# Kernel tuning notes

Measured on AMD Instinct MI355X. Metric: run time of the kernel, lower is better.

Reference implementation:

```python
import jax, jax.numpy as jnp
import numpy as np

D_MODEL = 256
N_HEADS = 8
D_HEAD = D_MODEL // N_HEADS
EMB = [16, 16, 16, 16]
CUMSUM = [0, 16, 32, 48, 64]
PSUM = sum(EMB)
LEVELS = [(122, 122), (61, 61), (31, 31), (16, 16)]
S_TOTAL = sum(h * w for h, w in LEVELS)
IMG = 976.0


def swap_pairs(x):
    # swap consecutive pairs along the leading (view) dim
    return x.reshape(-1, 2, *x.shape[1:])[:, ::-1].reshape(x.shape)


def grid_sample_bilinear(img, grid):
    # img: [B, H, W, D]; grid: [B, Q, 2] in [-1, 1]; align_corners=False, zero padding
    B, H, W, D = img.shape
    gx = (grid[..., 0] + 1.0) * (W * 0.5) - 0.5
    gy = (grid[..., 1] + 1.0) * (H * 0.5) - 0.5
    x0 = jnp.floor(gx)
    y0 = jnp.floor(gy)
    wx = (gx - x0)[..., None]
    wy = (gy - y0)[..., None]
    x0i = x0.astype(jnp.int32)
    y0i = y0.astype(jnp.int32)
    flat = img.reshape(B, H * W, D)

    def gather(xi, yi):
        valid = ((xi >= 0) & (xi < W) & (yi >= 0) & (yi < H)).astype(img.dtype)
        idx = jnp.clip(yi, 0, H - 1) * W + jnp.clip(xi, 0, W - 1)
        v = jnp.take_along_axis(flat, idx[..., None], axis=1)
        return v * valid[..., None]

    v00 = gather(x0i, y0i)
    v01 = gather(x0i + 1, y0i)
    v10 = gather(x0i, y0i + 1)
    v11 = gather(x0i + 1, y0i + 1)
    return (v00 * (1 - wx) * (1 - wy) + v01 * wx * (1 - wy)
            + v10 * (1 - wx) * wy + v11 * wx * wy)


def ms_deform_attn_core(value, shapes, sampling_locations, attention_weights):
    # value: [N, S, M, D]; sampling_locations: [N, Lq, M, P, 2]; attention_weights: [N, Lq, M, P]
    N, S, M, D = value.shape
    Lq = sampling_locations.shape[1]
    grids = 2.0 * sampling_locations - 1.0
    outs = []
    start = 0
    for lid, (H, W) in enumerate(shapes):
        p0, p1 = CUMSUM[lid], CUMSUM[lid + 1]
        Pl = p1 - p0
        v = value[:, start:start + H * W].reshape(N, H, W, M, D)
        v = v.transpose(0, 3, 1, 2, 4).reshape(N * M, H, W, D)
        g = grids[:, :, :, p0:p1].transpose(0, 2, 1, 3, 4).reshape(N * M, Lq * Pl, 2)
        outs.append(grid_sample_bilinear(v, g).reshape(N * M, Lq, Pl, D))
        start += H * W
    samp = jnp.concatenate(outs, axis=2)  # [N*M, Lq, Psum, D]
    w = attention_weights.transpose(0, 2, 1, 3).reshape(N * M, Lq, PSUM, 1)
    out = (samp * w).sum(axis=2)  # [N*M, Lq, D]
    return out.reshape(N, M, Lq, D).transpose(0, 2, 1, 3).reshape(N, Lq, M * D)


def _forward(query, input_flatten, reference_points, p_pfws, pt_transforms,
             W_val, b_val, W_attn, b_attn, W_out, b_out, shapes):
    N, Lq, _ = query.shape
    value = (input_flatten @ W_val.T + b_val).reshape(N, -1, N_HEADS, D_HEAD)
    attn = jax.nn.softmax((query @ W_attn.T + b_attn).reshape(N, Lq, N_HEADS, PSUM), axis=-1)

    # reverse 2x3 affine transform on reference points, scale to pixels
    A = pt_transforms[:, :, :2]
    t = pt_transforms[:, :, 2]
    orig = jnp.einsum('nij,nqj->nqi', jnp.linalg.inv(A), reference_points - t[:, None, :]) * IMG

    # epipolar line in the second (swapped) view: point(x) = ts + ms * x, x in [0, IMG]
    P1 = p_pfws
    P2 = swap_pairs(p_pfws)
    A1 = P1[:, :, :3]
    b1 = P1[:, :, 3]
    cam = -jnp.linalg.solve(A1, b1[:, :, None])[:, :, 0]  # camera center [N,3]
    uh = jnp.concatenate([orig, jnp.ones_like(orig[..., :1])], -1)
    ray = jnp.einsum('nij,nqj->nqi', jnp.linalg.inv(A1), uh - b1[:, None, :])  # [N,Q,3]

    def proj2(X):
        Xh = jnp.concatenate([X, jnp.ones_like(X[..., :1])], -1)
        y = jnp.einsum('nij,nqj->nqi', P2, Xh)
        return y[..., :2] / (y[..., 2:3] + 1e-8)

    ts = proj2(jnp.broadcast_to(cam[:, None, :], ray.shape))
    ms = (proj2(ray) - ts) / IMG

    locs = []
    for n_pts in EMB:
        xs = jnp.linspace(0.0, IMG, n_pts)
        locs.append(ts[:, :, None, :] + ms[:, :, None, :] * xs[None, None, :, None])
    loc = jnp.concatenate(locs, axis=2) / IMG  # [N, Lq, Psum, 2]

    T2 = swap_pairs(pt_transforms)
    loc = jnp.einsum('nij,nqpj->nqpi', T2[:, :, :2], loc) + T2[:, :, 2][:, None, None, :]
    loc = jnp.clip(loc, 0.0, 1.0)
    samp_loc = jnp.broadcast_to(loc[:, :, None, :, :], (N, Lq, N_HEADS, PSUM, 2))

    out = ms_deform_attn_core(swap_pairs(value), shapes, samp_loc, attn)
    return out @ W_out.T + b_out


def setup_inputs() -> dict:
    key = jax.random.key(0)
    ks = jax.random.split(key, 12)
    N, Lq = 4, 1000
    query = jax.random.normal(ks[0], (N, Lq, D_MODEL), jnp.float32)
    input_flatten = jax.random.normal(ks[1], (N, S_TOTAL, D_MODEL), jnp.float32)
    reference_points = jax.random.uniform(ks[2], (N, Lq, 2), jnp.float32)
    p_pfws = jnp.asarray(np.eye(3, 4), jnp.float32) + 0.05 * jax.random.normal(ks[3], (N, 3, 4), jnp.float32)
    pt_transforms = jnp.asarray(np.eye(2, 3), jnp.float32) + 0.05 * jax.random.normal(ks[4], (N, 2, 3), jnp.float32)
    W_val = 0.05 * jax.random.normal(ks[5], (D_MODEL, D_MODEL), jnp.float32)
    b_val = jnp.zeros((D_MODEL,), jnp.float32)
    W_attn = 0.05 * jax.random.normal(ks[6], (N_HEADS * PSUM, D_MODEL), jnp.float32)
    b_attn = jnp.zeros((N_HEADS * PSUM,), jnp.float32)
    W_out = 0.05 * jax.random.normal(ks[7], (D_MODEL, D_MODEL), jnp.float32)
    b_out = jnp.zeros((D_MODEL,), jnp.float32)
    input_spatial_shapes = np.asarray(LEVELS, np.int64)
    input_level_start_index = np.asarray(np.cumsum([0] + [h * w for h, w in LEVELS])[:-1], np.int64)
    return {"query": query, "input_flatten": input_flatten, "reference_points": reference_points,
            "p_pfws": p_pfws, "pt_transforms": pt_transforms,
            "W_val": W_val, "b_val": b_val, "W_attn": W_attn, "b_attn": b_attn,
            "W_out": W_out, "b_out": b_out,
            "input_spatial_shapes": input_spatial_shapes,
            "input_level_start_index": input_level_start_index}


def reference(query, input_flatten, reference_points, p_pfws, pt_transforms,
              W_val, b_val, W_attn, b_attn, W_out, b_out,
              input_spatial_shapes, input_level_start_index):
    shapes = [(int(h), int(w)) for h, w in np.asarray(input_spatial_shapes)]
    return _forward(query, input_flatten, reference_points, p_pfws, pt_transforms,
                    W_val, b_val, W_attn, b_attn, W_out, b_out, shapes)
```

## Files before the change

kernel.cpp:

```cpp
#include <hip/hip_runtime.h>
#include <hip/hip_bf16.h>
#include <math.h>

#define NB 4
#define LQ 1000
#define NHEAD 8
#define DHEAD 32
#define DMODEL 256
#define PSUM 64
#define STOT 19822
#define IMGF 976.0f
#define GK 256

__device__ __constant__ int c_LH[4] = {122, 61, 31, 16};
__device__ __constant__ int c_LW[4] = {122, 61, 31, 16};
__device__ __constant__ int c_LST[4] = {0, 14884, 18605, 19566};

typedef __attribute__((ext_vector_type(8))) short bf16x8;
typedef __attribute__((ext_vector_type(4))) float f32x4;

__device__ inline unsigned int pk2(float a, float b) {
    unsigned short ua = __bfloat16_as_ushort(__float2bfloat16(a));
    unsigned short ub = __bfloat16_as_ushort(__float2bfloat16(b));
    return (unsigned int)ua | ((unsigned int)ub << 16);
}
__device__ inline float bf2f(unsigned short u) {
    return __uint_as_float(((unsigned int)u) << 16);
}
__device__ inline bf16x8 cvt8(float4 u, float4 v) {
    union { unsigned int w[4]; bf16x8 h; } r;
    r.w[0] = pk2(u.x, u.y); r.w[1] = pk2(u.z, u.w);
    r.w[2] = pk2(v.x, v.y); r.w[3] = pk2(v.z, v.w);
    return r.h;
}
__device__ inline void gll16(const void* g, void* l) {
    __builtin_amdgcn_global_load_lds(
        (const __attribute__((address_space(1))) void*)g,
        (__attribute__((address_space(3))) void*)l, 16, 0, 0);
}
__device__ inline void hard_barrier() {
    asm volatile("" ::: "memory");
    __builtin_amdgcn_sched_barrier(0);
    __builtin_amdgcn_s_barrier();
    __builtin_amdgcn_sched_barrier(0);
    asm volatile("" ::: "memory");
}

__device__ inline void make_consts(int n, const float* p_pfws, const float* pt,
                                   float* consts) {
    const float* P1 = p_pfws + n * 12;
    const float* P2 = p_pfws + (n ^ 1) * 12;
    const float* T  = pt + n * 6;
    const float* T2 = pt + (n ^ 1) * 6;
    float* C = consts + n * 48;
    float det = T[0]*T[4] - T[1]*T[3];
    float idet = 1.0f/det;
    C[0] =  T[4]*idet; C[1] = -T[1]*idet;
    C[2] = -T[3]*idet; C[3] =  T[0]*idet;
    C[4] = T[2]; C[5] = T[5];
    float a=P1[0], b=P1[1], c=P1[2];
    float d=P1[4], e=P1[5], f=P1[6];
    float g=P1[8], h=P1[9], i=P1[10];
    float b10=P1[3], b11=P1[7], b12=P1[11];
    float A_=e*i-f*h, B_=c*h-b*i, Cc=b*f-c*e;
    float D_=f*g-d*i, E_=a*i-c*g, F_=c*d-a*f;
    float G_=d*h-e*g, H_=b*g-a*h, I_=a*e-b*d;
    float det3 = a*A_ + b*D_ + c*G_;
    float id3 = 1.0f/det3;
    C[6]=A_*id3;  C[7]=B_*id3;  C[8]=Cc*id3;
    C[9]=D_*id3;  C[10]=E_*id3; C[11]=F_*id3;
    C[12]=G_*id3; C[13]=H_*id3; C[14]=I_*id3;
    C[15]=b10; C[16]=b11; C[17]=b12;
    for (int k = 0; k < 12; ++k) C[18+k] = P2[k];
    float cam0 = -(C[6]*b10  + C[7]*b11  + C[8]*b12);
    float cam1 = -(C[9]*b10  + C[10]*b11 + C[11]*b12);
    float cam2 = -(C[12]*b10 + C[13]*b11 + C[14]*b12);
    float y0 = P2[0]*cam0 + P2[1]*cam1 + P2[2]*cam2  + P2[3];
    float y1 = P2[4]*cam0 + P2[5]*cam1 + P2[6]*cam2  + P2[7];
    float y2 = P2[8]*cam0 + P2[9]*cam1 + P2[10]*cam2 + P2[11];
    float inv = 1.0f/(y2 + 1e-8f);
    C[30] = y0*inv; C[31] = y1*inv;
    for (int k = 0; k < 6; ++k) C[32+k] = T2[k];
}

__global__ void prep(const float* __restrict__ Wv, const float* __restrict__ Wa,
                     const float* __restrict__ Wo,
                     unsigned short* __restrict__ wbv, unsigned short* __restrict__ wba,
                     unsigned short* __restrict__ wbo,
                     const float* __restrict__ p_pfws, const float* __restrict__ pt,
                     float* __restrict__ consts) {
    int bid = blockIdx.x;
    if (bid == 256) {
        int n = threadIdx.x;
        if (n < NB) make_consts(n, p_pfws, pt, consts);
        return;
    }
    int i = bid * 256 + threadIdx.x;
    const float* src; unsigned short* dst; int off;
    if (i < 16384)      { src = Wv; dst = wbv; off = i; }
    else if (i < 49152) { src = Wa; dst = wba; off = i - 16384; }
    else                { src = Wo; dst = wbo; off = i - 49152; }
    float4 f = ((const float4*)src)[off];
    ushort4 o;
    o.x = __bfloat16_as_ushort(__float2bfloat16(f.x));
    o.y = __bfloat16_as_ushort(__float2bfloat16(f.y));
    o.z = __bfloat16_as_ushort(__float2bfloat16(f.z));
    o.w = __bfloat16_as_ushort(__float2bfloat16(f.w));
    ((ushort4*)dst)[off] = o;
}

__global__ __launch_bounds__(256, 1)
void gemm_val_regB(const float* __restrict__ X, const unsigned short* __restrict__ Wb,
                   const float* __restrict__ bias, unsigned short* __restrict__ out,
                   int M, int T, int CHUNK) {
    __shared__ __align__(16) char As[2][32768];
    const int tid  = threadIdx.x;
    const int lane = tid & 63;
    const int wq   = tid >> 6;
    const int l15  = lane & 15;
    const int koct = lane >> 4;
    const int t0   = blockIdx.x * CHUNK;
    int nt = T - t0; if (nt > CHUNK) nt = CHUNK;
    if (nt <= 0) return;

    bf16x8 breg[8][4];
    #pragma unroll
    for (int ks = 0; ks < 8; ++ks)
        #pragma unroll
        for (int ni = 0; ni < 4; ++ni) {
            int col = wq * 64 + ni * 16 + l15;
            breg[ks][ni] = *(const bf16x8*)((const char*)Wb + (size_t)col * 512
                                            + ks * 64 + koct * 16);
        }
    float bias_v[4];
    #pragma unroll
    for (int ni = 0; ni < 4; ++ni) bias_v[ni] = bias[wq * 64 + ni * 16 + l15];

#define STAGE(g, b) do {                                                      \
        _Pragma("unroll") for (int j = 0; j < 8; ++j) {                       \
            int r_ = wq * 8 + j;                                              \
            int gr_ = (g) * 32 + r_; if (gr_ >= M) gr_ = M - 1;               \
            int lch_ = lane ^ (r_ & 7);                                       \
            gll16(X + (size_t)gr_ * GK + lch_ * 4, As[b] + r_ * 1024);        \
        } } while (0)

    STAGE(t0, 0);
    if (nt > 1) { STAGE(t0 + 1, 1); asm volatile("s_waitcnt vmcnt(8)" ::: "memory"); }
    else        {                   asm volatile("s_waitcnt vmcnt(0)" ::: "memory"); }
    hard_barrier();

#define COMPUTE_STORE(g, b) do {                                              \
        f32x4 acc[2][4] = {};                                                 \
        _Pragma("unroll") for (int ks = 0; ks < 8; ++ks) {                    \
            _Pragma("unroll") for (int mi = 0; mi < 2; ++mi) {                \
                int r_ = mi * 16 + l15;                                       \
                int ch_ = ks * 8 + koct * 2;                                  \
                float4 x0_ = *(const float4*)(As[b] + r_ * 1024 +             \
                                              ((ch_    ) ^ (r_ & 7)) * 16);   \
                float4 x1_ = *(const float4*)(As[b] + r_ * 1024 +             \
                                              ((ch_ + 1) ^ (r_ & 7)) * 16);   \
                bf16x8 af_ = cvt8(x0_, x1_);                                  \
                _Pragma("unroll") for (int ni = 0; ni < 4; ++ni)              \
                    acc[mi][ni] = __builtin_amdgcn_mfma_f32_16x16x32_bf16(    \
                        af_, breg[ks][ni], acc[mi][ni], 0, 0, 0);             \
            }                                                                 \
        }                                                                     \
        _Pragma("unroll") for (int mi = 0; mi < 2; ++mi) {                    \
            int rb_ = (g) * 32 + mi * 16 + (lane >> 4) * 4;                   \
            _Pragma("unroll") for (int j_ = 0; j_ < 4; ++j_) {                \
                int gr_ = rb_ + j_;                                           \
                if (gr_ < M) {                                                \
                    _Pragma("unroll") for (int ni = 0; ni < 4; ++ni)          \
                        out[(size_t)gr_ * DMODEL + wq * 64 + ni * 16 + l15] = \
                            __bfloat16_as_ushort(__float2bfloat16(            \
                                acc[mi][ni][j_] + bias_v[ni]));               \
                }                                                             \
            }                                                                 \
        } } while (0)

    for (int t = 0; t < nt; ++t) {
        COMPUTE_STORE(t0 + t, t & 1);
        if (t + 1 == nt) break;
        hard_barrier();
        if (t + 2 < nt) {
            STAGE(t0 + t + 2, t & 1);
            asm volatile("s_waitcnt vmcnt(40)" ::: "memory");
        } else {
            asm volatile("s_waitcnt vmcnt(32)" ::: "memory");
        }
        hard_barrier();
    }
#undef COMPUTE_STORE
#undef STAGE
}

template<bool OUT_BF16>
__global__ __launch_bounds__(256, 4)
void gemm64(const float* __restrict__ A, const unsigned short* __restrict__ Bb,
            const float* __restrict__ bias, void* __restrict__ outp,
            int M, int N) {
    __shared__ char smem[40960];
    char* asmem = smem;
    char* bsmem = smem + 8192;
    const int tid  = threadIdx.x;
    const int lane = tid & 63;
    const int w    = tid >> 6;
    const int l15  = lane & 15;
    const int koct = lane >> 4;
    const int i0 = blockIdx.x * 64;
    const int o0 = blockIdx.y * 256;

    const int s_row = tid >> 2;
    const int s_q   = tid & 3;
    int gr = i0 + s_row; gr = gr < M ? gr : M - 1;
    const float* aptr = A + (size_t)gr * GK + s_q * 16;
    const int s_sw = (s_row & 7) << 4;
    char* a_w0 = asmem + s_row * 128 + ((s_q * 32)      ^ s_sw);
    char* a_w1 = asmem + s_row * 128 + ((s_q * 32 + 16) ^ s_sw);

    const int b_sub = lane >> 3;
    const int b_kc  = (lane & 7) ^ b_sub;

    f32x4 acc[4][4] = {};
    float bias_v[4];
    #pragma unroll
    for (int ni = 0; ni < 4; ++ni) bias_v[ni] = bias[o0 + w * 64 + ni * 16 + l15];

    for (int t = 0; t < 4; ++t) {
        const int k0 = t * 64;
        #pragma unroll
        for (int j = 0; j < 8; ++j) {
            int cI = w * 8 + j;
            int col = cI * 8 + b_sub;
            gll16(Bb + (size_t)(o0 + col) * GK + k0 + b_kc * 8,
                  bsmem + cI * 1024);
        }
        {
            const float4* s = (const float4*)(aptr + k0);
            float4 f0 = s[0], f1 = s[1], f2 = s[2], f3 = s[3];
            uint4 wv0, wv1;
            wv0.x = pk2(f0.x,f0.y); wv0.y = pk2(f0.z,f0.w);
            wv0.z = pk2(f1.x,f1.y); wv0.w = pk2(f1.z,f1.w);
            wv1.x = pk2(f2.x,f2.y); wv1.y = pk2(f2.z,f2.w);
            wv1.z = pk2(f3.x,f3.y); wv1.w = pk2(f3.z,f3.w);
            *(uint4*)a_w0 = wv0;
            *(uint4*)a_w1 = wv1;
        }
        __syncthreads();
        #pragma unroll
        for (int ks = 0; ks < 2; ++ks) {
            const int kc = ks * 4 + koct;
            bf16x8 af[4], bfr[4];
            #pragma unroll
            for (int mi = 0; mi < 4; ++mi) {
                int r = mi * 16 + l15;
                af[mi] = *(const bf16x8*)(asmem + r * 128 + ((kc * 16) ^ ((r & 7) << 4)));
            }
            #pragma unroll
            for (int ni = 0; ni < 4; ++ni) {
                int c = w * 64 + ni * 16 + l15;
                bfr[ni] = *(const bf16x8*)(bsmem + c * 128 + ((kc * 16) ^ ((c & 7) << 4)));
            }
            #pragma unroll
            for (int mi = 0; mi < 4; ++mi)
                #pragma unroll
                for (int ni = 0; ni < 4; ++ni)
                    acc[mi][ni] = __builtin_amdgcn_mfma_f32_16x16x32_bf16(
                        af[mi], bfr[ni], acc[mi][ni], 0, 0, 0);
        }
        __syncthreads();
    }

    #pragma unroll
    for (int mi = 0; mi < 4; ++mi) {
        int rbase = i0 + mi * 16 + (lane >> 4) * 4;
        #pragma unroll
        for (int j = 0; j < 4; ++j) {
            int grow = rbase + j;
            if (grow < M) {
                #pragma unroll
                for (int ni = 0; ni < 4; ++ni) {
                    int gcol = o0 + w * 64 + ni * 16 + l15;
                    float v = acc[mi][ni][j] + bias_v[ni];
                    if (OUT_BF16)
                        ((unsigned short*)outp)[(size_t)grow * N + gcol] =
                            __bfloat16_as_ushort(__float2bfloat16(v));
                    else
                        ((float*)outp)[(size_t)grow * N + gcol] = v;
                }
            }
        }
    }
}

__global__ __launch_bounds__(256)
void fused_sample(const float* __restrict__ logits,
                  const float* __restrict__ ref_pts,
                  const unsigned short* __restrict__ value,
                  const float* __restrict__ consts,
                  float* __restrict__ attn_out) {
    int b = blockIdx.x;
    int n = b / LQ;
    int q = b - n * LQ;
    int tid = threadIdx.x;

    __shared__ float s_attn[512];
    __shared__ float s_loc[16][2];
    __shared__ int   s_idx[64][4];
    __shared__ float s_w[64][4];
    __shared__ float4 s_part[4][64];

    s_attn[tid]       = logits[(size_t)b * 512 + tid];
    s_attn[tid + 256] = logits[(size_t)b * 512 + tid + 256];
    __syncthreads();

    {
        int wave = tid >> 6, lane = tid & 63;
        for (int h = wave; h < NHEAD; h += 4) {
            float v = s_attn[h * 64 + lane];
            float mx = v;
            #pragma unroll
            for (int off = 32; off; off >>= 1) mx = fmaxf(mx, __shfl_xor(mx, off, 64));
            float e = expf(v - mx);
            float sm = e;
            #pragma unroll
            for (int off = 32; off; off >>= 1) sm += __shfl_xor(sm, off, 64);
            s_attn[h * 64 + lane] = e / sm;
        }
    }

    if (tid < 16) {
        const float* C = consts + n * 48;
        float rx = ref_pts[((size_t)n * LQ + q) * 2 + 0];
        float ry = ref_pts[((size_t)n * LQ + q) * 2 + 1];
        float dx = rx - C[4], dy = ry - C[5];
        float ox = (C[0]*dx + C[1]*dy) * IMGF;
        float oy = (C[2]*dx + C[3]*dy) * IMGF;
        float u0 = ox - C[15], u1 = oy - C[16], u2 = 1.0f - C[17];
        float r0 = C[6]*u0  + C[7]*u1  + C[8]*u2;
        float r1 = C[9]*u0  + C[10]*u1 + C[11]*u2;
        float r2 = C[12]*u0 + C[13]*u1 + C[14]*u2;
        float y0 = C[18]*r0 + C[19]*r1 + C[20]*r2 + C[21];
        float y1 = C[22]*r0 + C[23]*r1 + C[24]*r2 + C[25];
        float y2 = C[26]*r0 + C[27]*r1 + C[28]*r2 + C[29];
        float inv = 1.0f/(y2 + 1e-8f);
        float prx = y0*inv, pry = y1*inv;
        float ts0 = C[30], ts1 = C[31];
        float msx = (prx - ts0) / IMGF, msy = (pry - ts1) / IMGF;
        int j = tid;
        float xsj = IMGF * ((float)j / 15.0f);
        float lx = (ts0 + msx * xsj) / IMGF;
        float ly = (ts1 + msy * xsj) / IMGF;
        float Lx = C[32]*lx + C[33]*ly + C[34];
        float Ly = C[35]*lx + C[36]*ly + C[37];
        s_loc[j][0] = fminf(fmaxf(Lx, 0.0f), 1.0f);
        s_loc[j][1] = fminf(fmaxf(Ly, 0.0f), 1.0f);
    }
    __syncthreads();

    if (tid < 64) {
        int p = tid, lev = p >> 4, j = p & 15;
        int H = c_LH[lev], W = c_LW[lev], st = c_LST[lev];
        float gx = s_loc[j][0] * (float)W - 0.5f;
        float gy = s_loc[j][1] * (float)H - 0.5f;
        float x0f = floorf(gx), y0f = floorf(gy);
        float wx = gx - x0f, wy = gy - y0f;
        int x0 = (int)x0f, y0 = (int)y0f;
        int x1 = x0 + 1, y1 = y0 + 1;
        bool vx0 = (x0 >= 0) & (x0 < W), vx1 = (x1 >= 0) & (x1 < W);
        bool vy0 = (y0 >= 0) & (y0 < H), vy1 = (y1 >= 0) & (y1 < H);
        s_idx[p][0] = (vx0 & vy0) ? st + y0 * W + x0 : -1;  s_w[p][0] = (1.f-wx)*(1.f-wy);
        s_idx[p][1] = (vx1 & vy0) ? st + y0 * W + x1 : -1;  s_w[p][1] = wx*(1.f-wy);
        s_idx[p][2] = (vx0 & vy1) ? st + y1 * W + x0 : -1;  s_w[p][2] = (1.f-wx)*wy;
        s_idx[p][3] = (vx1 & vy1) ? st + y1 * W + x1 : -1;  s_w[p][3] = wx*wy;
    }
    __syncthreads();

    int wv = tid >> 6, lane = tid & 63;
    const unsigned short* vbase = value + (size_t)(n ^ 1) * STOT * DMODEL + lane * 4;
    int m = lane >> 3;
    float a0 = 0.f, a1 = 0.f, a2 = 0.f, a3 = 0.f;
    #pragma unroll 4
    for (int j = 0; j < 16; ++j) {
        int p = wv * 16 + j;
        float wa = s_attn[m * 64 + p];
        float s0 = 0.f, s1 = 0.f, s2 = 0.f, s3 = 0.f;
        #pragma unroll
        for (int cc = 0; cc < 4; ++cc) {
            int idx = s_idx[p][cc];
            if (idx >= 0) {
                ushort4 vv = *(const ushort4*)(vbase + (size_t)idx * DMODEL);
                float wgt = s_w[p][cc];
                s0 += wgt * bf2f(vv.x);
                s1 += wgt * bf2f(vv.y);
                s2 += wgt * bf2f(vv.z);
                s3 += wgt * bf2f(vv.w);
            }
        }
        a0 += wa * s0; a1 += wa * s1; a2 += wa * s2; a3 += wa * s3;
    }
    s_part[wv][lane] = make_float4(a0, a1, a2, a3);
    __syncthreads();

    const float* sp = (const float*)s_part;
    float r = sp[tid] + sp[256 + tid] + sp[512 + tid] + sp[768 + tid];
    attn_out[(size_t)b * DMODEL + tid] = r;
}

extern "C" void kernel_launch(void* const* d_in, const int* in_sizes, int n_in,
                              void* d_out, int out_size, void* d_ws, size_t ws_size,
                              hipStream_t stream) {
    const float* query         = (const float*)d_in[0];
    const float* input_flatten = (const float*)d_in[1];
    const float* ref_pts       = (const float*)d_in[2];
    const float* p_pfws        = (const float*)d_in[3];
    const float* pt            = (const float*)d_in[4];
    const float* W_val         = (const float*)d_in[5];
    const float* b_val         = (const float*)d_in[6];
    const float* W_attn        = (const float*)d_in[7];
    const float* b_attn        = (const float*)d_in[8];
    const float* W_out         = (const float*)d_in[9];
    const float* b_out         = (const float*)d_in[10];
    float* out = (float*)d_out;

    const int M = NB * STOT;
    const size_t value_bytes  = (size_t)M * DMODEL * 2;
    const size_t logits_bytes = (size_t)NB * LQ * 512 * 4;
    const size_t attn_bytes   = (size_t)NB * LQ * DMODEL * 4;
    const size_t consts_bytes = NB * 48 * 4;
    const size_t wv_bytes     = (size_t)DMODEL * DMODEL * 2;
    const size_t wa_bytes     = (size_t)512 * DMODEL * 2;
    const size_t wo_bytes     = (size_t)DMODEL * DMODEL * 2;
    const size_t need = value_bytes + logits_bytes + attn_bytes + consts_bytes
                      + wv_bytes + wa_bytes + wo_bytes;
    if (ws_size < need) return;

    char* p = (char*)d_ws;
    unsigned short* value = (unsigned short*)p;  p += value_bytes;
    float* logits   = (float*)p;                 p += logits_bytes;
    float* attn_out = (float*)p;                 p += attn_bytes;
    float* consts   = (float*)p;                 p += consts_bytes;
    unsigned short* wb_val  = (unsigned short*)p; p += wv_bytes;
    unsigned short* wb_attn = (unsigned short*)p; p += wa_bytes;
    unsigned short* wb_out  = (unsigned short*)p; p += wo_bytes;

    prep<<<257, 256, 0, stream>>>(W_val, W_attn, W_out, wb_val, wb_attn, wb_out,
                                  p_pfws, pt, consts);

    {
        const int T = (M + 31) / 32;
        const int CHUNK = 5;
        const int blocks = (T + CHUNK - 1) / CHUNK;
        gemm_val_regB<<<blocks, 256, 0, stream>>>(input_flatten, wb_val, b_val,
                                                  value, M, T, CHUNK);
    }
    {
        dim3 g((NB * LQ + 63) / 64, 2);
        gemm64<false><<<g, 256, 0, stream>>>(query, wb_attn, b_attn, logits, NB * LQ, 512);
    }
    fused_sample<<<NB * LQ, 256, 0, stream>>>(logits, ref_pts, value, consts, attn_out);
    {
        dim3 g((NB * LQ + 63) / 64, 1);
        gemm64<false><<<g, 256, 0, stream>>>(attn_out, wb_out, b_out, out, NB * LQ, DMODEL);
    }
}
```

Measured before the change: 94.00 us.

## Split sampling points across two blocks per query and sum partials in output GEMM

The sampling kernel now launches two 128-thread blocks per query. Each block handles half of the 64 sampling points and writes its partial sum to a separate buffer, and the output projection GEMM adds the two partial buffers while loading A. The aim is more, smaller blocks for better occupancy and latency hiding in the gather-heavy stage. The cost is that each block repeats the softmax and location setup, and the partial buffers add extra global writes and reads. An empty asm barrier is also added on the weight register loads in the value GEMM to control scheduling.

```diff
diff --git a/kernel.cpp b/kernel.cpp
--- a/kernel.cpp
+++ b/kernel.cpp
@@ -125,13 +125,16 @@
 
     bf16x8 breg[8][4];
     #pragma unroll
-    for (int ks = 0; ks < 8; ++ks)
+    for (int ks = 0; ks < 8; ++ks) {
         #pragma unroll
         for (int ni = 0; ni < 4; ++ni) {
             int col = wq * 64 + ni * 16 + l15;
             breg[ks][ni] = *(const bf16x8*)((const char*)Wb + (size_t)col * 512
                                             + ks * 64 + koct * 16);
         }
+        asm volatile("" : "+v"(breg[ks][0]), "+v"(breg[ks][1]),
+                          "+v"(breg[ks][2]), "+v"(breg[ks][3]));
+    }
     float bias_v[4];
     #pragma unroll
     for (int ni = 0; ni < 4; ++ni) bias_v[ni] = bias[wq * 64 + ni * 16 + l15];
@@ -194,9 +197,10 @@
 #undef STAGE
 }
 
-template<bool OUT_BF16>
+template<bool OUT_BF16, bool SUM2>
 __global__ __launch_bounds__(256, 4)
-void gemm64(const float* __restrict__ A, const unsigned short* __restrict__ Bb,
+void gemm64(const float* __restrict__ A, const float* __restrict__ A2,
+            const unsigned short* __restrict__ Bb,
             const float* __restrict__ bias, void* __restrict__ outp,
             int M, int N) {
     __shared__ char smem[40960];
@@ -213,7 +217,8 @@
     const int s_row = tid >> 2;
     const int s_q   = tid & 3;
     int gr = i0 + s_row; gr = gr < M ? gr : M - 1;
-    const float* aptr = A + (size_t)gr * GK + s_q * 16;
+    const float* aptr  = A  + (size_t)gr * GK + s_q * 16;
+    const float* aptr2 = SUM2 ? (A2 + (size_t)gr * GK + s_q * 16) : nullptr;
     const int s_sw = (s_row & 7) << 4;
     char* a_w0 = asmem + s_row * 128 + ((s_q * 32)      ^ s_sw);
     char* a_w1 = asmem + s_row * 128 + ((s_q * 32 + 16) ^ s_sw);
@@ -238,6 +243,14 @@
         {
             const float4* s = (const float4*)(aptr + k0);
             float4 f0 = s[0], f1 = s[1], f2 = s[2], f3 = s[3];
+            if (SUM2) {
+                const float4* s2 = (const float4*)(aptr2 + k0);
+                float4 g0 = s2[0], g1 = s2[1], g2 = s2[2], g3 = s2[3];
+                f0.x += g0.x; f0.y += g0.y; f0.z += g0.z; f0.w += g0.w;
+                f1.x += g1.x; f1.y += g1.y; f1.z += g1.z; f1.w += g1.w;
+                f2.x += g2.x; f2.y += g2.y; f2.z += g2.z; f2.w += g2.w;
+                f3.x += g3.x; f3.y += g3.y; f3.z += g3.z; f3.w += g3.w;
+            }
             uint4 wv0, wv1;
             wv0.x = pk2(f0.x,f0.y); wv0.y = pk2(f0.z,f0.w);
             wv0.z = pk2(f1.x,f1.y); wv0.w = pk2(f1.z,f1.w);
@@ -293,30 +306,33 @@
     }
 }
 
-__global__ __launch_bounds__(256)
+__global__ __launch_bounds__(128)
 void fused_sample(const float* __restrict__ logits,
                   const float* __restrict__ ref_pts,
                   const unsigned short* __restrict__ value,
                   const float* __restrict__ consts,
-                  float* __restrict__ attn_out) {
+                  float* __restrict__ pp0,
+                  float* __restrict__ pp1) {
     int b = blockIdx.x;
+    int half = blockIdx.y;
     int n = b / LQ;
     int q = b - n * LQ;
     int tid = threadIdx.x;
 
     __shared__ float s_attn[512];
     __shared__ float s_loc[16][2];
-    __shared__ int   s_idx[64][4];
-    __shared__ float s_w[64][4];
-    __shared__ float4 s_part[4][64];
-
-    s_attn[tid]       = logits[(size_t)b * 512 + tid];
-    s_attn[tid + 256] = logits[(size_t)b * 512 + tid + 256];
+    __shared__ int   s_idx[32][4];
+    __shared__ float s_w[32][4];
+    __shared__ float4 s_part[2][64];
+
+    #pragma unroll
+    for (int r = 0; r < 4; ++r)
+        s_attn[tid + r * 128] = logits[(size_t)b * 512 + tid + r * 128];
     __syncthreads();
 
     {
         int wave = tid >> 6, lane = tid & 63;
-        for (int h = wave; h < NHEAD; h += 4) {
+        for (int h = wave; h < NHEAD; h += 2) {
             float v = s_attn[h * 64 + lane];
             float mx = v;
             #pragma unroll
@@ -358,8 +374,9 @@
     }
     __syncthreads();
 
-    if (tid < 64) {
-        int p = tid, lev = p >> 4, j = p & 15;
+    if (tid < 32) {
+        int p = half * 32 + tid;
+        int lev = p >> 4, j = p & 15;
         int H = c_LH[lev], W = c_LW[lev], st = c_LST[lev];
         float gx = s_loc[j][0] * (float)W - 0.5f;
         float gy = s_loc[j][1] * (float)H - 0.5f;
@@ -369,10 +386,10 @@
         int x1 = x0 + 1, y1 = y0 + 1;
         bool vx0 = (x0 >= 0) & (x0 < W), vx1 = (x1 >= 0) & (x1 < W);
         bool vy0 = (y0 >= 0) & (y0 < H), vy1 = (y1 >= 0) & (y1 < H);
-        s_idx[p][0] = (vx0 & vy0) ? st + y0 * W + x0 : -1;  s_w[p][0] = (1.f-wx)*(1.f-wy);
-        s_idx[p][1] = (vx1 & vy0) ? st + y0 * W + x1 : -1;  s_w[p][1] = wx*(1.f-wy);
-        s_idx[p][2] = (vx0 & vy1) ? st + y1 * W + x0 : -1;  s_w[p][2] = (1.f-wx)*wy;
-        s_idx[p][3] = (vx1 & vy1) ? st + y1 * W + x1 : -1;  s_w[p][3] = wx*wy;
+        s_idx[tid][0] = (vx0 & vy0) ? st + y0 * W + x0 : -1;  s_w[tid][0] = (1.f-wx)*(1.f-wy);
+        s_idx[tid][1] = (vx1 & vy0) ? st + y0 * W + x1 : -1;  s_w[tid][1] = wx*(1.f-wy);
+        s_idx[tid][2] = (vx0 & vy1) ? st + y1 * W + x0 : -1;  s_w[tid][2] = (1.f-wx)*wy;
+        s_idx[tid][3] = (vx1 & vy1) ? st + y1 * W + x1 : -1;  s_w[tid][3] = wx*wy;
     }
     __syncthreads();
 
@@ -382,15 +399,16 @@
     float a0 = 0.f, a1 = 0.f, a2 = 0.f, a3 = 0.f;
     #pragma unroll 4
     for (int j = 0; j < 16; ++j) {
-        int p = wv * 16 + j;
+        int lp = wv * 16 + j;
+        int p  = half * 32 + lp;
         float wa = s_attn[m * 64 + p];
         float s0 = 0.f, s1 = 0.f, s2 = 0.f, s3 = 0.f;
         #pragma unroll
         for (int cc = 0; cc < 4; ++cc) {
-            int idx = s_idx[p][cc];
+            int idx = s_idx[lp][cc];
             if (idx >= 0) {
                 ushort4 vv = *(const ushort4*)(vbase + (size_t)idx * DMODEL);
-                float wgt = s_w[p][cc];
+                float wgt = s_w[lp][cc];
                 s0 += wgt * bf2f(vv.x);
                 s1 += wgt * bf2f(vv.y);
                 s2 += wgt * bf2f(vv.z);
@@ -402,9 +420,10 @@
     s_part[wv][lane] = make_float4(a0, a1, a2, a3);
     __syncthreads();
 
+    float* pp = half ? pp1 : pp0;
     const float* sp = (const float*)s_part;
-    float r = sp[tid] + sp[256 + tid] + sp[512 + tid] + sp[768 + tid];
-    attn_out[(size_t)b * DMODEL + tid] = r;
+    pp[(size_t)b * DMODEL + tid]       = sp[tid]       + sp[256 + tid];
+    pp[(size_t)b * DMODEL + tid + 128] = sp[tid + 128] + sp[384 + tid];
 }
 
 extern "C" void kernel_launch(void* const* d_in, const int* in_sizes, int n_in,
@@ -426,19 +445,20 @@
     const int M = NB * STOT;
     const size_t value_bytes  = (size_t)M * DMODEL * 2;
     const size_t logits_bytes = (size_t)NB * LQ * 512 * 4;
-    const size_t attn_bytes   = (size_t)NB * LQ * DMODEL * 4;
+    const size_t pp_bytes     = (size_t)NB * LQ * DMODEL * 4;
     const size_t consts_bytes = NB * 48 * 4;
     const size_t wv_bytes     = (size_t)DMODEL * DMODEL * 2;
     const size_t wa_bytes     = (size_t)512 * DMODEL * 2;
     const size_t wo_bytes     = (size_t)DMODEL * DMODEL * 2;
-    const size_t need = value_bytes + logits_bytes + attn_bytes + consts_bytes
+    const size_t need = value_bytes + logits_bytes + 2 * pp_bytes + consts_bytes
                       + wv_bytes + wa_bytes + wo_bytes;
     if (ws_size < need) return;
 
     char* p = (char*)d_ws;
     unsigned short* value = (unsigned short*)p;  p += value_bytes;
     float* logits   = (float*)p;                 p += logits_bytes;
-    float* attn_out = (float*)p;                 p += attn_bytes;
+    float* pp0      = (float*)p;                 p += pp_bytes;
+    float* pp1      = (float*)p;                 p += pp_bytes;
     float* consts   = (float*)p;                 p += consts_bytes;
     unsigned short* wb_val  = (unsigned short*)p; p += wv_bytes;
     unsigned short* wb_attn = (unsigned short*)p; p += wa_bytes;
@@ -456,11 +476,16 @@
     }
     {
         dim3 g((NB * LQ + 63) / 64, 2);
-        gemm64<false><<<g, 256, 0, stream>>>(query, wb_attn, b_attn, logits, NB * LQ, 512);
-    }
-    fused_sample<<<NB * LQ, 256, 0, stream>>>(logits, ref_pts, value, consts, attn_out);
+        gemm64<false, false><<<g, 256, 0, stream>>>(query, nullptr, wb_attn, b_attn,
+                                                    logits, NB * LQ, 512);
+    }
+    {
+        dim3 g(NB * LQ, 2);
+        fused_sample<<<g, 128, 0, stream>>>(logits, ref_pts, value, consts, pp0, pp1);
+    }
     {
         dim3 g((NB * LQ + 63) / 64, 1);
-        gemm64<false><<<g, 256, 0, stream>>>(attn_out, wb_out, b_out, out, NB * LQ, DMODEL);
-    }
-}
+        gemm64<false, true><<<g, 256, 0, stream>>>(pp0, pp1, wb_out, b_out,
+                                                   out, NB * LQ, DMODEL);
+    }
+}
```

New measurement: 101.2 us. 7.7% more time.

## Split sampling blocks by channel half and map value batches to XCDs

Applied to the files above, without the earlier changes.

The fused sampling kernel now launches two 128-thread blocks per query, each covering half the channels (four heads). Block IDs are decoded so that each XCD (bid & 7) always handles the same value batch and channel half, which aims to keep the gathered value rows resident in that XCD's L2. The sampling loop loads 2 bf16 per lane instead of 4 and each wave covers 32 points. A separate empty asm barrier pins the preloaded B fragments in the value GEMM, presumably to control when those register loads are scheduled. Costs are smaller per-lane loads and per-block coordinate and softmax work that is now duplicated across the two halves.

```diff
diff --git a/kernel.cpp b/kernel.cpp
--- a/kernel.cpp
+++ b/kernel.cpp
@@ -125,13 +125,16 @@
 
     bf16x8 breg[8][4];
     #pragma unroll
-    for (int ks = 0; ks < 8; ++ks)
+    for (int ks = 0; ks < 8; ++ks) {
         #pragma unroll
         for (int ni = 0; ni < 4; ++ni) {
             int col = wq * 64 + ni * 16 + l15;
             breg[ks][ni] = *(const bf16x8*)((const char*)Wb + (size_t)col * 512
                                             + ks * 64 + koct * 16);
         }
+        asm volatile("" : "+v"(breg[ks][0]), "+v"(breg[ks][1]),
+                          "+v"(breg[ks][2]), "+v"(breg[ks][3]));
+    }
     float bias_v[4];
     #pragma unroll
     for (int ni = 0; ni < 4; ++ni) bias_v[ni] = bias[wq * 64 + ni * 16 + l15];
@@ -293,31 +296,35 @@
     }
 }
 
-__global__ __launch_bounds__(256)
+__global__ __launch_bounds__(128)
 void fused_sample(const float* __restrict__ logits,
                   const float* __restrict__ ref_pts,
                   const unsigned short* __restrict__ value,
                   const float* __restrict__ consts,
                   float* __restrict__ attn_out) {
-    int b = blockIdx.x;
-    int n = b / LQ;
-    int q = b - n * LQ;
-    int tid = threadIdx.x;
-
-    __shared__ float s_attn[512];
+    const int bid = blockIdx.x;
+    const int xcd   = bid & 7;
+    const int gb    = xcd >> 1;
+    const int chalf = xcd & 1;
+    const int q     = bid >> 3;
+    const int n     = gb ^ 1;
+    const int row   = n * LQ + q;
+    const int tid = threadIdx.x;
+
+    __shared__ float s_attn[256];
     __shared__ float s_loc[16][2];
     __shared__ int   s_idx[64][4];
     __shared__ float s_w[64][4];
-    __shared__ float4 s_part[4][64];
-
-    s_attn[tid]       = logits[(size_t)b * 512 + tid];
-    s_attn[tid + 256] = logits[(size_t)b * 512 + tid + 256];
+    __shared__ float s_red[2][128];
+
+    s_attn[tid]       = logits[(size_t)row * 512 + chalf * 256 + tid];
+    s_attn[tid + 128] = logits[(size_t)row * 512 + chalf * 256 + tid + 128];
     __syncthreads();
 
     {
         int wave = tid >> 6, lane = tid & 63;
-        for (int h = wave; h < NHEAD; h += 4) {
-            float v = s_attn[h * 64 + lane];
+        for (int hl = wave; hl < 4; hl += 2) {
+            float v = s_attn[hl * 64 + lane];
             float mx = v;
             #pragma unroll
             for (int off = 32; off; off >>= 1) mx = fmaxf(mx, __shfl_xor(mx, off, 64));
@@ -325,7 +332,7 @@
             float sm = e;
             #pragma unroll
             for (int off = 32; off; off >>= 1) sm += __shfl_xor(sm, off, 64);
-            s_attn[h * 64 + lane] = e / sm;
+            s_attn[hl * 64 + lane] = e / sm;
         }
     }
 
@@ -377,34 +384,33 @@
     __syncthreads();
 
     int wv = tid >> 6, lane = tid & 63;
-    const unsigned short* vbase = value + (size_t)(n ^ 1) * STOT * DMODEL + lane * 4;
-    int m = lane >> 3;
-    float a0 = 0.f, a1 = 0.f, a2 = 0.f, a3 = 0.f;
+    const unsigned short* vbase = value + (size_t)gb * STOT * DMODEL
+                                + chalf * 128 + lane * 2;
+    int hl = lane >> 4;
+    float a0 = 0.f, a1 = 0.f;
     #pragma unroll 4
-    for (int j = 0; j < 16; ++j) {
-        int p = wv * 16 + j;
-        float wa = s_attn[m * 64 + p];
-        float s0 = 0.f, s1 = 0.f, s2 = 0.f, s3 = 0.f;
+    for (int j = 0; j < 32; ++j) {
+        int p = wv * 32 + j;
+        float wa = s_attn[hl * 64 + p];
+        float s0 = 0.f, s1 = 0.f;
         #pragma unroll
         for (int cc = 0; cc < 4; ++cc) {
             int idx = s_idx[p][cc];
             if (idx >= 0) {
-                ushort4 vv = *(const ushort4*)(vbase + (size_t)idx * DMODEL);
+                unsigned int vv = *(const unsigned int*)(vbase + (size_t)idx * DMODEL);
                 float wgt = s_w[p][cc];
-                s0 += wgt * bf2f(vv.x);
-                s1 += wgt * bf2f(vv.y);
-                s2 += wgt * bf2f(vv.z);
-                s3 += wgt * bf2f(vv.w);
+                s0 += wgt * bf2f((unsigned short)(vv & 0xffff));
+                s1 += wgt * bf2f((unsigned short)(vv >> 16));
             }
         }
-        a0 += wa * s0; a1 += wa * s1; a2 += wa * s2; a3 += wa * s3;
-    }
-    s_part[wv][lane] = make_float4(a0, a1, a2, a3);
+        a0 += wa * s0; a1 += wa * s1;
+    }
+    s_red[wv][lane * 2]     = a0;
+    s_red[wv][lane * 2 + 1] = a1;
     __syncthreads();
 
-    const float* sp = (const float*)s_part;
-    float r = sp[tid] + sp[256 + tid] + sp[512 + tid] + sp[768 + tid];
-    attn_out[(size_t)b * DMODEL + tid] = r;
+    attn_out[(size_t)row * DMODEL + chalf * 128 + tid] =
+        s_red[0][tid] + s_red[1][tid];
 }
 
 extern "C" void kernel_launch(void* const* d_in, const int* in_sizes, int n_in,
@@ -458,7 +464,10 @@
         dim3 g((NB * LQ + 63) / 64, 2);
         gemm64<false><<<g, 256, 0, stream>>>(query, wb_attn, b_attn, logits, NB * LQ, 512);
     }
-    fused_sample<<<NB * LQ, 256, 0, stream>>>(logits, ref_pts, value, consts, attn_out);
+    {
+        fused_sample<<<NB * LQ * 2, 128, 0, stream>>>(logits, ref_pts, value,
+                                                      consts, attn_out);
+    }
     {
         dim3 g((NB * LQ + 63) / 64, 1);
         gemm64<false><<<g, 256, 0, stream>>>(attn_out, wb_out, b_out, out, NB * LQ, DMODEL);
```

After: 105.0 us. 1.12x slower.
